# Performance work log

Measured on AMD Instinct MI355X. Metric: run time of the kernel, lower is better.

## Reference

```python
import jax, jax.numpy as jnp
import numpy as np

N_STEPS = 2048; WINDOW = [4, 4, 4]; INNER = 5
D_MODEL = 128; N_HEADS = 4; D_K = D_MODEL // N_HEADS
D_FFN = 512; N_LAYERS = 2; D_BOT = D_MODEL // 4; BATCH = 2
NEG = -1e9


def _mask_and_sizes():
    # faithful port of Pyraformer get_mask
    all_size = [N_STEPS]
    for w in WINDOW:
        all_size.append(all_size[-1] // w)
    S = sum(all_size)
    m = np.zeros((S, S), np.float32)
    inner = INNER // 2
    starts = [0]
    for sz in all_size:
        starts.append(starts[-1] + sz)
    for li, sz in enumerate(all_size):
        s = starts[li]
        for i in range(s, s + sz):
            m[i, max(i - inner, s):min(i + inner + 1, s + sz)] = 1
    for li in range(1, len(all_size)):
        s = starts[li]
        for i in range(s, s + all_size[li]):
            left = (s - all_size[li - 1]) + (i - s) * WINDOW[li - 1]
            right = s if i == s + all_size[li] - 1 else (s - all_size[li - 1]) + (i - s + 1) * WINDOW[li - 1]
            m[i, left:right] = 1
            m[left:right, i] = 1
    return (1 - m).astype(bool), all_size  # True = masked out


def _refer_points(all_size):
    # faithful port of Pyraformer refer_points -> [n_steps, n_levels]
    idx = np.zeros((N_STEPS, len(all_size)), np.int32)
    for i in range(N_STEPS):
        idx[i, 0] = i
        former = i
        for j in range(1, len(all_size)):
            start = int(sum(all_size[:j]))
            inner_idx = former - (start - all_size[j - 1])
            former = start + min(inner_idx // WINDOW[j - 1], all_size[j] - 1)
            idx[i, j] = former
    return idx


def _ln(x, g, b, eps):
    mu = jnp.mean(x, -1, keepdims=True)
    var = jnp.mean((x - mu) ** 2, -1, keepdims=True)
    return (x - mu) * jax.lax.rsqrt(var + eps) * g + b


def setup_inputs() -> dict:
    key = jax.random.key(0)
    ks = jax.random.split(key, 12)
    mask_np, all_size = _mask_and_sizes()
    idx_np = _refer_points(all_size)
    s = 0.02
    rn = lambda k, shape: jax.random.normal(k, shape, jnp.float32) * s
    L, W = N_LAYERS, len(WINDOW)
    return {
        'x': jax.random.normal(ks[0], (BATCH, N_STEPS, D_MODEL), jnp.float32),
        'w_down': rn(ks[1], (D_MODEL, D_BOT)), 'b_down': jnp.zeros((D_BOT,)),
        'conv_w': rn(ks[2], (W, D_BOT, D_BOT, WINDOW[0])), 'conv_b': jnp.zeros((W, D_BOT)),
        'bn_g': jnp.ones((W, D_BOT)), 'bn_b': jnp.zeros((W, D_BOT)),
        'bn_m': jnp.zeros((W, D_BOT)), 'bn_v': jnp.ones((W, D_BOT)),
        'w_up': rn(ks[3], (D_BOT, D_MODEL)), 'b_up': jnp.zeros((D_MODEL,)),
        'ln0_g': jnp.ones((D_MODEL,)), 'ln0_b': jnp.zeros((D_MODEL,)),
        'wq': rn(ks[4], (L, D_MODEL, N_HEADS * D_K)), 'wk': rn(ks[5], (L, D_MODEL, N_HEADS * D_K)),
        'wv': rn(ks[6], (L, D_MODEL, N_HEADS * D_K)), 'wo': rn(ks[7], (L, N_HEADS * D_K, D_MODEL)),
        'ln1_g': jnp.ones((L, D_MODEL)), 'ln1_b': jnp.zeros((L, D_MODEL)),
        'ffn_w1': rn(ks[8], (L, D_MODEL, D_FFN)), 'ffn_b1': jnp.zeros((L, D_FFN)),
        'ffn_w2': rn(ks[9], (L, D_FFN, D_MODEL)), 'ffn_b2': jnp.zeros((L, D_MODEL)),
        'ln2_g': jnp.ones((L, D_MODEL)), 'ln2_b': jnp.zeros((L, D_MODEL)),
        'mask': jnp.asarray(mask_np), 'indexes': jnp.asarray(idx_np),
    }


def _fwd(mask, indexes, x, w_down, b_down, conv_w, conv_b, bn_g, bn_b, bn_m, bn_v,
         w_up, b_up, ln0_g, ln0_b, wq, wk, wv, wo, ln1_g, ln1_b,
         ffn_w1, ffn_b1, ffn_w2, ffn_b2, ln2_g, ln2_b):
    B = x.shape[0]
    # Bottleneck_Construct: down-proj, strided convs per scale, up-proj, concat, LN
    t = (x @ w_down + b_down).transpose(0, 2, 1)  # [B, d_bot, N]
    outs = []
    for i in range(len(WINDOW)):
        t = jax.lax.conv_general_dilated(t, conv_w[i], (WINDOW[i],), 'VALID',
                                         dimension_numbers=('NCH', 'OIH', 'NCH'))
        t = t + conv_b[i][None, :, None]
        t = (t - bn_m[i][None, :, None]) * jax.lax.rsqrt(bn_v[i][None, :, None] + 1e-5) \
            * bn_g[i][None, :, None] + bn_b[i][None, :, None]  # BatchNorm1d (eval)
        t = jax.nn.elu(t)
        outs.append(t)
    pooled = jnp.concatenate(outs, axis=2).transpose(0, 2, 1)  # [B, 672, d_bot]
    h = jnp.concatenate([x, pooled @ w_up + b_up], axis=1)  # [B, S=2720, d_model]
    h = _ln(h, ln0_g, ln0_b, 1e-5)
    S = h.shape[1]
    mask4 = mask[None, None]  # [1,1,S,S], True = masked
    inv_temp = 1.0 / np.float32(np.sqrt(D_K))
    for l in range(N_LAYERS):
        q = (h @ wq[l]).reshape(B, S, N_HEADS, D_K).transpose(0, 2, 1, 3)
        k = (h @ wk[l]).reshape(B, S, N_HEADS, D_K).transpose(0, 2, 1, 3)
        v = (h @ wv[l]).reshape(B, S, N_HEADS, D_K).transpose(0, 2, 1, 3)
        attn = jnp.einsum('bhqd,bhkd->bhqk', q * inv_temp, k)
        attn = jnp.where(mask4, NEG, attn)
        attn = jax.nn.softmax(attn, axis=-1)
        o = jnp.einsum('bhqk,bhkd->bhqd', attn, v).transpose(0, 2, 1, 3).reshape(B, S, N_HEADS * D_K)
        h = _ln(h + o @ wo[l], ln1_g[l], ln1_b[l], 1e-6)
        f = jax.nn.relu(h @ ffn_w1[l] + ffn_b1[l]) @ ffn_w2[l] + ffn_b2[l]
        h = _ln(h + f, ln2_g[l], ln2_b[l], 1e-6)
    # multi-scale gather reassembly (refer_points)
    idx_flat = indexes.reshape(-1)  # [n_steps * n_levels]
    all_enc = h[:, idx_flat, :]  # [B, n_steps*levels, d_model]
    return all_enc.reshape(B, N_STEPS, -1)  # [B, n_steps, levels*d_model]


def reference(x, mask, indexes, w_down, b_down, conv_w, conv_b, bn_g, bn_b, bn_m, bn_v,
              w_up, b_up, ln0_g, ln0_b, wq, wk, wv, wo, ln1_g, ln1_b,
              ffn_w1, ffn_b1, ffn_w2, ffn_b2, ln2_g, ln2_b):
    return _fwd(mask, indexes, x, w_down, b_down, conv_w, conv_b, bn_g, bn_b, bn_m, bn_v,
                w_up, b_up, ln0_g, ln0_b, wq, wk, wv, wo, ln1_g, ln1_b,
                ffn_w1, ffn_b1, ffn_w2, ffn_b2, ln2_g, ln2_b)
```

## Files before the change

### kernel.cpp

```cpp
#include <hip/hip_runtime.h>
#include <hip/hip_bf16.h>

#define S_TOT 2720

typedef short bf16x8 __attribute__((ext_vector_type(8)));
typedef float f32x4 __attribute__((ext_vector_type(4)));

__device__ __forceinline__ float bf2f(short u) {
    return __uint_as_float(((unsigned int)(unsigned short)u) << 16);
}

__global__ void prep_kernel(const float* __restrict__ w1, const float* __restrict__ w2,
                            const float* __restrict__ wq, const float* __restrict__ wk,
                            const float* __restrict__ wv, const float* __restrict__ wo,
                            __hip_bfloat16* __restrict__ out,
                            const float* __restrict__ x, const float* __restrict__ wd,
                            const float* __restrict__ bd, float* __restrict__ t0) {
    int id = blockIdx.x * 256 + threadIdx.x;
    if (id < 131072) {
        int l = id >> 16, r = id & 65535;
        int j = r >> 7, k = r & 127;
        out[id] = __float2bfloat16(w1[l * 65536 + k * 512 + j]);
    } else if (id < 262144) {
        int t = id - 131072;
        int l = t >> 16, r = t & 65535;
        int d = r >> 9, j = r & 511;
        out[id] = __float2bfloat16(w2[l * 65536 + j * 128 + d]);
    } else if (id < 360448) {
        int t = id - 262144;
        int l = t / 49152, r = t % 49152;
        int m = r >> 14, rr = r & 16383;
        int j = rr >> 7, k = rr & 127;
        const float* W = (m == 0) ? wq : (m == 1) ? wk : wv;
        out[id] = __float2bfloat16(W[l * 16384 + k * 128 + j]);
    } else if (id < 393216) {
        int t = id - 360448;
        int l = t >> 14, r = t & 16383;
        int j = r >> 7, k = r & 127;
        out[id] = __float2bfloat16(wo[l * 16384 + k * 128 + j]);
    } else {
        int did = id - 393216;
        int c = did & 31;
        int r = did >> 5;
        const float* xr = x + (size_t)r * 128;
        float a0 = bd[c], a1 = 0.f, a2 = 0.f, a3 = 0.f;
#pragma unroll
        for (int k = 0; k < 128; k += 4) {
            a0 += xr[k]     * wd[(k)     * 32 + c];
            a1 += xr[k + 1] * wd[(k + 1) * 32 + c];
            a2 += xr[k + 2] * wd[(k + 2) * 32 + c];
            a3 += xr[k + 3] * wd[(k + 3) * 32 + c];
        }
        t0[did] = (a0 + a1) + (a2 + a3);
    }
}

__global__ void conv_kernel(const float* __restrict__ in, float* __restrict__ pooled,
                            const float* __restrict__ cw, const float* __restrict__ cb,
                            const float* __restrict__ bg, const float* __restrict__ bb,
                            const float* __restrict__ bm, const float* __restrict__ bv,
                            int level, int in_bstride, int in_off, int Lout, int out_off,
                            int total) {
    int id = blockIdx.x * 256 + threadIdx.x;
    if (id >= total) return;
    int co = id & 31;
    int lo = (id >> 5) % Lout;
    int b  = id / (32 * Lout);
    const float* ib = in + (size_t)(b * in_bstride + in_off + lo * 4) * 32;
    const float* w  = cw + (size_t)(level * 32 + co) * 32 * 4;
    float acc0 = 0.f, acc1 = 0.f, acc2 = 0.f, acc3 = 0.f;
#pragma unroll
    for (int ci = 0; ci < 32; ++ci) {
        acc0 += ib[0 * 32 + ci] * w[ci * 4 + 0];
        acc1 += ib[1 * 32 + ci] * w[ci * 4 + 1];
        acc2 += ib[2 * 32 + ci] * w[ci * 4 + 2];
        acc3 += ib[3 * 32 + ci] * w[ci * 4 + 3];
    }
    float acc = ((acc0 + acc1) + (acc2 + acc3)) + cb[level * 32 + co];
    acc = (acc - bm[level * 32 + co]) * rsqrtf(bv[level * 32 + co] + 1e-5f)
          * bg[level * 32 + co] + bb[level * 32 + co];
    acc = acc > 0.f ? acc : expm1f(acc);
    pooled[(size_t)(b * 672 + out_off + lo) * 32 + co] = acc;
}

__global__ void build_ln_kernel(const float* __restrict__ x, const float* __restrict__ pooled,
                                const float* __restrict__ w_up, const float* __restrict__ b_up,
                                const float* __restrict__ g, const float* __restrict__ bta,
                                float* __restrict__ h) {
    int wave = threadIdx.x >> 6;
    int lane = threadIdx.x & 63;
    int row = blockIdx.x * 4 + wave;
    int b = row / S_TOT, s = row % S_TOT;
    float v0, v1;
    if (s < 2048) {
        const float* xr = x + (size_t)(b * 2048 + s) * 128;
        v0 = xr[lane]; v1 = xr[lane + 64];
    } else {
        int p = s - 2048;
        const float* pr = pooled + (size_t)(b * 672 + p) * 32;
        float a0 = b_up[lane], a1 = b_up[lane + 64];
        float a2 = 0.f, a3 = 0.f;
#pragma unroll
        for (int k = 0; k < 32; k += 2) {
            float p0 = pr[k], p1 = pr[k + 1];
            a0 += p0 * w_up[k * 128 + lane];
            a1 += p0 * w_up[k * 128 + lane + 64];
            a2 += p1 * w_up[(k + 1) * 128 + lane];
            a3 += p1 * w_up[(k + 1) * 128 + lane + 64];
        }
        v0 = a0 + a2; v1 = a1 + a3;
    }
    float sum = v0 + v1;
#pragma unroll
    for (int off = 32; off; off >>= 1) sum += __shfl_xor(sum, off);
    float mu = sum * (1.f / 128.f);
    float d0 = v0 - mu, d1 = v1 - mu;
    float vs = d0 * d0 + d1 * d1;
#pragma unroll
    for (int off = 32; off; off >>= 1) vs += __shfl_xor(vs, off);
    float inv = rsqrtf(vs * (1.f / 128.f) + 1e-5f);
    h[(size_t)row * 128 + lane]      = d0 * inv * g[lane]      + bta[lane];
    h[(size_t)row * 128 + lane + 64] = d1 * inv * g[lane + 64] + bta[lane + 64];
}

__global__ __launch_bounds__(256) void qkv_mfma_kernel(const float* __restrict__ H,
                                                       const __hip_bfloat16* __restrict__ wqkvt,
                                                       __hip_bfloat16* __restrict__ q,
                                                       __hip_bfloat16* __restrict__ k,
                                                       __hip_bfloat16* __restrict__ v) {
    __shared__ __hip_bfloat16 hsb[16][136];
    int tid = threadIdx.x;
    int r0 = blockIdx.x * 16;
    {
        int row = tid >> 4, c0 = (tid & 15) * 8;
        const float* src = &H[(size_t)(r0 + row) * 128 + c0];
        float4 x0 = *(const float4*)src;
        float4 x1 = *(const float4*)(src + 4);
        __hip_bfloat16* d = &hsb[row][c0];
        d[0] = __float2bfloat16(x0.x); d[1] = __float2bfloat16(x0.y);
        d[2] = __float2bfloat16(x0.z); d[3] = __float2bfloat16(x0.w);
        d[4] = __float2bfloat16(x1.x); d[5] = __float2bfloat16(x1.y);
        d[6] = __float2bfloat16(x1.z); d[7] = __float2bfloat16(x1.w);
    }
    __syncthreads();
    int lane = tid & 63, wv = tid >> 6;
    int l15 = lane & 15, grp = lane >> 4;
    bf16x8 afr[4];
#pragma unroll
    for (int ks = 0; ks < 4; ++ks)
        afr[ks] = *(const bf16x8*)&hsb[l15][ks * 32 + grp * 8];
    __hip_bfloat16* O[3] = {q, k, v};
#pragma unroll
    for (int t = 0; t < 6; ++t) {
        int gt = wv * 6 + t;
        int mat = gt >> 3, jj = gt & 7;
        int j0 = jj * 16;
        f32x4 acc = {0.f, 0.f, 0.f, 0.f};
        const __hip_bfloat16* wb = &wqkvt[(size_t)(mat * 128 + j0 + l15) * 128 + grp * 8];
#pragma unroll
        for (int ks = 0; ks < 4; ++ks) {
            bf16x8 bfr = *(const bf16x8*)&wb[ks * 32];
            acc = __builtin_amdgcn_mfma_f32_16x16x32_bf16(afr[ks], bfr, acc, 0, 0, 0);
        }
        __hip_bfloat16* Om = O[mat];
#pragma unroll
        for (int i = 0; i < 4; ++i)
            Om[(size_t)(r0 + grp * 4 + i) * 128 + j0 + l15] = __float2bfloat16(acc[i]);
    }
}

__global__ __launch_bounds__(256) void attn_o_ffn_kernel(const __hip_bfloat16* __restrict__ Q,
                                                         const __hip_bfloat16* __restrict__ K,
                                                         const __hip_bfloat16* __restrict__ V,
                                                         const __hip_bfloat16* __restrict__ wot,
                                                         const float* __restrict__ g1,
                                                         const float* __restrict__ b1ta,
                                                         const __hip_bfloat16* __restrict__ w1t,
                                                         const float* __restrict__ b1,
                                                         const __hip_bfloat16* __restrict__ w2t,
                                                         const float* __restrict__ b2,
                                                         const float* __restrict__ g2,
                                                         const float* __restrict__ b2ta,
                                                         float* __restrict__ h) {
    __shared__ __hip_bfloat16 osb[16][136];
    __shared__ __hip_bfloat16 pb[16][520];
    __shared__ float partf[16][128];
    __shared__ float h1s[16][128];
    int tid = threadIdx.x;
    int r0 = blockIdx.x * 16;
    {
        int rl = tid >> 4;
        int hh = (tid >> 2) & 3;
        int qd = tid & 3;
        int d0 = qd * 8;
        int row = r0 + rl;
        int b = row / S_TOT, i = row % S_TOT;
        int li, s;
        if (i < 2048)      { li = 0; s = 0;    }
        else if (i < 2560) { li = 1; s = 2048; }
        else if (i < 2688) { li = 2; s = 2560; }
        else               { li = 3; s = 2688; }
        int sz = (li == 0) ? 2048 : (li == 1) ? 512 : (li == 2) ? 128 : 32;
        int pstart = (li == 0) ? 2048 : (li == 1) ? 2560 : 2688;
        int cstart = (li == 1) ? 0 : (li == 2) ? 2048 : 2560;

        bf16x8 qv = *(const bf16x8*)(Q + (size_t)row * 128 + hh * 32 + d0);
        float qf[8];
#pragma unroll
        for (int e = 0; e < 8; ++e) qf[e] = bf2f(qv[e]);
        const float invt = 0.17677669529663687f;

        float sc[10];
        int   nj[10];
        bool  vl[10];
#pragma unroll
        for (int slot = 0; slot < 10; ++slot) {
            int j; bool valid;
            if (slot < 5)       { j = i - 2 + slot;                         valid = (j >= s) && (j < s + sz); }
            else if (slot == 5) { j = pstart + ((i - s) >> 2);              valid = (li < 3); }
            else                { j = cstart + ((i - s) << 2) + (slot - 6); valid = (li > 0); }
            nj[slot] = j; vl[slot] = valid;
            float dot = 0.f;
            if (valid) {
                bf16x8 kv = *(const bf16x8*)(K + (size_t)(b * S_TOT + j) * 128 + hh * 32 + d0);
#pragma unroll
                for (int e = 0; e < 8; ++e) dot += qf[e] * bf2f(kv[e]);
            }
            dot += __shfl_xor(dot, 1);
            dot += __shfl_xor(dot, 2);
            sc[slot] = valid ? dot * invt : -1e30f;
        }
        float mx = sc[0];
#pragma unroll
        for (int slot = 1; slot < 10; ++slot) mx = fmaxf(mx, sc[slot]);
        float ssum = 0.f;
#pragma unroll
        for (int slot = 0; slot < 10; ++slot) { sc[slot] = __expf(sc[slot] - mx); ssum += sc[slot]; }
        float rinv = 1.f / ssum;
        float oacc[8];
#pragma unroll
        for (int e = 0; e < 8; ++e) oacc[e] = 0.f;
#pragma unroll
        for (int slot = 0; slot < 10; ++slot) {
            if (vl[slot]) {
                float p = sc[slot] * rinv;
                bf16x8 vv = *(const bf16x8*)(V + (size_t)(b * S_TOT + nj[slot]) * 128 + hh * 32 + d0);
#pragma unroll
                for (int e = 0; e < 8; ++e) oacc[e] += p * bf2f(vv[e]);
            }
        }
        __hip_bfloat16* dst = &osb[rl][hh * 32 + d0];
#pragma unroll
        for (int e = 0; e < 8; ++e) dst[e] = __float2bfloat16(oacc[e]);
    }
    __syncthreads();
    int lane = tid & 63, wv = tid >> 6;
    int l15 = lane & 15, grp = lane >> 4;
    {
        bf16x8 afr[4];
#pragma unroll
        for (int ks = 0; ks < 4; ++ks)
            afr[ks] = *(const bf16x8*)&osb[l15][ks * 32 + grp * 8];
#pragma unroll
        for (int t = 0; t < 2; ++t) {
            int j0 = (wv * 2 + t) * 16;
            f32x4 acc = {0.f, 0.f, 0.f, 0.f};
            const __hip_bfloat16* wb = &wot[(size_t)(j0 + l15) * 128 + grp * 8];
#pragma unroll
            for (int ks = 0; ks < 4; ++ks) {
                bf16x8 bfr = *(const bf16x8*)&wb[ks * 32];
                acc = __builtin_amdgcn_mfma_f32_16x16x32_bf16(afr[ks], bfr, acc, 0, 0, 0);
            }
#pragma unroll
            for (int i = 0; i < 4; ++i)
                partf[grp * 4 + i][j0 + l15] = acc[i];
        }
    }
    __syncthreads();
    {
        int r = tid >> 4, d0 = (tid & 15) * 8;
        size_t row = (size_t)(r0 + r) * 128;
        float vv[8];
        float sum = 0.f;
#pragma unroll
        for (int i = 0; i < 8; ++i) {
            int d = d0 + i;
            vv[i] = partf[r][d] + h[row + d];
            sum += vv[i];
        }
#pragma unroll
        for (int off = 8; off; off >>= 1) sum += __shfl_xor(sum, off);
        float mu = sum * (1.f / 128.f);
        float vs = 0.f;
#pragma unroll
        for (int i = 0; i < 8; ++i) { vv[i] -= mu; vs += vv[i] * vv[i]; }
#pragma unroll
        for (int off = 8; off; off >>= 1) vs += __shfl_xor(vs, off);
        float inv = rsqrtf(vs * (1.f / 128.f) + 1e-6f);
        __hip_bfloat16* db = &osb[r][d0];
#pragma unroll
        for (int i = 0; i < 8; ++i) {
            float hv = vv[i] * inv * g1[d0 + i] + b1ta[d0 + i];
            h1s[r][d0 + i] = hv;
            db[i] = __float2bfloat16(hv);
        }
    }
    __syncthreads();
    {
        bf16x8 afr[4];
#pragma unroll
        for (int ks = 0; ks < 4; ++ks)
            afr[ks] = *(const bf16x8*)&osb[l15][ks * 32 + grp * 8];
#pragma unroll
        for (int t = 0; t < 8; ++t) {
            int j0 = (wv * 8 + t) * 16;
            f32x4 acc = {0.f, 0.f, 0.f, 0.f};
            const __hip_bfloat16* wb = &w1t[(size_t)(j0 + l15) * 128 + grp * 8];
#pragma unroll
            for (int ks = 0; ks < 4; ++ks) {
                bf16x8 bfr = *(const bf16x8*)&wb[ks * 32];
                acc = __builtin_amdgcn_mfma_f32_16x16x32_bf16(afr[ks], bfr, acc, 0, 0, 0);
            }
            float bv = b1[j0 + l15];
#pragma unroll
            for (int i = 0; i < 4; ++i)
                pb[grp * 4 + i][j0 + l15] = __float2bfloat16(fmaxf(acc[i] + bv, 0.f));
        }
    }
    __syncthreads();
    {
        f32x4 acc2a = {0.f, 0.f, 0.f, 0.f};
        f32x4 acc2b = {0.f, 0.f, 0.f, 0.f};
        const __hip_bfloat16* wb0 = &w2t[(size_t)(wv * 32 + l15) * 512 + grp * 8];
        const __hip_bfloat16* wb1 = &w2t[(size_t)(wv * 32 + 16 + l15) * 512 + grp * 8];
#pragma unroll
        for (int ks = 0; ks < 16; ++ks) {
            bf16x8 afr2 = *(const bf16x8*)&pb[l15][ks * 32 + grp * 8];
            bf16x8 b0 = *(const bf16x8*)&wb0[ks * 32];
            bf16x8 b1f = *(const bf16x8*)&wb1[ks * 32];
            acc2a = __builtin_amdgcn_mfma_f32_16x16x32_bf16(afr2, b0, acc2a, 0, 0, 0);
            acc2b = __builtin_amdgcn_mfma_f32_16x16x32_bf16(afr2, b1f, acc2b, 0, 0, 0);
        }
#pragma unroll
        for (int i = 0; i < 4; ++i) {
            partf[grp * 4 + i][wv * 32 + l15]      = acc2a[i];
            partf[grp * 4 + i][wv * 32 + 16 + l15] = acc2b[i];
        }
    }
    __syncthreads();
    {
        int r = tid >> 4, d0 = (tid & 15) * 8;
        size_t row = (size_t)(r0 + r) * 128;
        float vv[8];
        float sum = 0.f;
#pragma unroll
        for (int i = 0; i < 8; ++i) {
            int d = d0 + i;
            vv[i] = partf[r][d] + b2[d] + h1s[r][d];
            sum += vv[i];
        }
#pragma unroll
        for (int off = 8; off; off >>= 1) sum += __shfl_xor(sum, off);
        float mu = sum * (1.f / 128.f);
        float vs = 0.f;
#pragma unroll
        for (int i = 0; i < 8; ++i) { vv[i] -= mu; vs += vv[i] * vv[i]; }
#pragma unroll
        for (int off = 8; off; off >>= 1) vs += __shfl_xor(vs, off);
        float inv = rsqrtf(vs * (1.f / 128.f) + 1e-6f);
#pragma unroll
        for (int i = 0; i < 8; ++i) vv[i] = vv[i] * inv * g2[d0 + i] + b2ta[d0 + i];
        *(float4*)&h[row + d0]     = make_float4(vv[0], vv[1], vv[2], vv[3]);
        *(float4*)&h[row + d0 + 4] = make_float4(vv[4], vv[5], vv[6], vv[7]);
    }
}

__global__ void gather_kernel(const float* __restrict__ H, const int* __restrict__ idx,
                              float* __restrict__ out) {
    int id = blockIdx.x * 256 + threadIdx.x;
    int d4 = id & 31;
    int j = (id >> 5) & 3;
    int t = (id >> 7) & 2047;
    int b = id >> 18;
    int src = idx[t * 4 + j];
    ((float4*)out)[id] = *(const float4*)&H[((size_t)(b * S_TOT + src) * 128) + d4 * 4];
}

extern "C" void kernel_launch(void* const* d_in, const int* in_sizes, int n_in,
                              void* d_out, int out_size, void* d_ws, size_t ws_size,
                              hipStream_t stream) {
    (void)in_sizes; (void)n_in; (void)out_size; (void)ws_size;
    const float* x       = (const float*)d_in[0];
    const float* w_down  = (const float*)d_in[1];
    const float* b_down  = (const float*)d_in[2];
    const float* conv_w  = (const float*)d_in[3];
    const float* conv_b  = (const float*)d_in[4];
    const float* bn_g    = (const float*)d_in[5];
    const float* bn_b    = (const float*)d_in[6];
    const float* bn_m    = (const float*)d_in[7];
    const float* bn_v    = (const float*)d_in[8];
    const float* w_up    = (const float*)d_in[9];
    const float* b_up    = (const float*)d_in[10];
    const float* ln0_g   = (const float*)d_in[11];
    const float* ln0_b   = (const float*)d_in[12];
    const float* wq      = (const float*)d_in[13];
    const float* wk      = (const float*)d_in[14];
    const float* wv      = (const float*)d_in[15];
    const float* wo      = (const float*)d_in[16];
    const float* ln1_g   = (const float*)d_in[17];
    const float* ln1_b   = (const float*)d_in[18];
    const float* ffn_w1  = (const float*)d_in[19];
    const float* ffn_b1  = (const float*)d_in[20];
    const float* ffn_w2  = (const float*)d_in[21];
    const float* ffn_b2  = (const float*)d_in[22];
    const float* ln2_g   = (const float*)d_in[23];
    const float* ln2_b   = (const float*)d_in[24];
    const int* indexes   = (const int*)d_in[26];

    float* ws = (float*)d_ws;
    float* t0     = ws;
    float* pooled = ws + 131072;
    float* h      = ws + 174080;
    __hip_bfloat16* qb = (__hip_bfloat16*)(ws + 870400);
    __hip_bfloat16* kb = (__hip_bfloat16*)(ws + 1218560);
    __hip_bfloat16* vb = (__hip_bfloat16*)(ws + 1566720);
    __hip_bfloat16* wb_all = (__hip_bfloat16*)(ws + 1914880);
    __hip_bfloat16* w1t   = wb_all;
    __hip_bfloat16* w2t   = wb_all + 131072;
    __hip_bfloat16* wqkvt = wb_all + 262144;
    __hip_bfloat16* wot   = wb_all + 360448;

    prep_kernel<<<2048, 256, 0, stream>>>(ffn_w1, ffn_w2, wq, wk, wv, wo, wb_all,
                                          x, w_down, b_down, t0);
    conv_kernel<<<128, 256, 0, stream>>>(t0, pooled, conv_w, conv_b, bn_g, bn_b, bn_m, bn_v,
                                         0, 2048, 0, 512, 0, 32768);
    conv_kernel<<<32, 256, 0, stream>>>(pooled, pooled, conv_w, conv_b, bn_g, bn_b, bn_m, bn_v,
                                        1, 672, 0, 128, 512, 8192);
    conv_kernel<<<8, 256, 0, stream>>>(pooled, pooled, conv_w, conv_b, bn_g, bn_b, bn_m, bn_v,
                                       2, 672, 512, 32, 640, 2048);
    build_ln_kernel<<<1360, 256, 0, stream>>>(x, pooled, w_up, b_up, ln0_g, ln0_b, h);

    for (int l = 0; l < 2; ++l) {
        qkv_mfma_kernel<<<340, 256, 0, stream>>>(h, wqkvt + l * 49152, qb, kb, vb);
        attn_o_ffn_kernel<<<340, 256, 0, stream>>>(qb, kb, vb, wot + l * 16384,
                                                   ln1_g + l * 128, ln1_b + l * 128,
                                                   w1t + l * 65536, ffn_b1 + l * 512,
                                                   w2t + l * 65536, ffn_b2 + l * 128,
                                                   ln2_g + l * 128, ln2_b + l * 128, h);
    }
    gather_kernel<<<2048, 256, 0, stream>>>(h, indexes, (float*)d_out);
}
```

Measured before the change: 115.7 us.

## Fuse small conv levels and fuse build-LN into first QKV projection

Merges the second and third pyramid conv levels into a single two-block kernel that keeps the intermediate level in shared memory. Fuses the input build and LayerNorm step into the first layer's QKV MFMA kernel, so the normalized rows feed the projection directly without re-reading h. This removes several kernel launches and a global round trip. The fused conv kernel runs on only two blocks with long serial loops, which may lengthen that stage.

```diff
diff --git a/kernel.cpp b/kernel.cpp
--- a/kernel.cpp
+++ b/kernel.cpp
@@ -83,44 +83,145 @@
     pooled[(size_t)(b * 672 + out_off + lo) * 32 + co] = acc;
 }
 
-__global__ void build_ln_kernel(const float* __restrict__ x, const float* __restrict__ pooled,
-                                const float* __restrict__ w_up, const float* __restrict__ b_up,
-                                const float* __restrict__ g, const float* __restrict__ bta,
-                                float* __restrict__ h) {
-    int wave = threadIdx.x >> 6;
-    int lane = threadIdx.x & 63;
-    int row = blockIdx.x * 4 + wave;
-    int b = row / S_TOT, s = row % S_TOT;
-    float v0, v1;
-    if (s < 2048) {
-        const float* xr = x + (size_t)(b * 2048 + s) * 128;
-        v0 = xr[lane]; v1 = xr[lane + 64];
-    } else {
-        int p = s - 2048;
-        const float* pr = pooled + (size_t)(b * 672 + p) * 32;
-        float a0 = b_up[lane], a1 = b_up[lane + 64];
-        float a2 = 0.f, a3 = 0.f;
-#pragma unroll
-        for (int k = 0; k < 32; k += 2) {
-            float p0 = pr[k], p1 = pr[k + 1];
-            a0 += p0 * w_up[k * 128 + lane];
-            a1 += p0 * w_up[k * 128 + lane + 64];
-            a2 += p1 * w_up[(k + 1) * 128 + lane];
-            a3 += p1 * w_up[(k + 1) * 128 + lane + 64];
-        }
-        v0 = a0 + a2; v1 = a1 + a3;
-    }
-    float sum = v0 + v1;
-#pragma unroll
-    for (int off = 32; off; off >>= 1) sum += __shfl_xor(sum, off);
-    float mu = sum * (1.f / 128.f);
-    float d0 = v0 - mu, d1 = v1 - mu;
-    float vs = d0 * d0 + d1 * d1;
-#pragma unroll
-    for (int off = 32; off; off >>= 1) vs += __shfl_xor(vs, off);
-    float inv = rsqrtf(vs * (1.f / 128.f) + 1e-5f);
-    h[(size_t)row * 128 + lane]      = d0 * inv * g[lane]      + bta[lane];
-    h[(size_t)row * 128 + lane + 64] = d1 * inv * g[lane + 64] + bta[lane + 64];
+__global__ __launch_bounds__(256) void conv23_kernel(float* __restrict__ pooled,
+                                                     const float* __restrict__ cw,
+                                                     const float* __restrict__ cb,
+                                                     const float* __restrict__ bg,
+                                                     const float* __restrict__ bb,
+                                                     const float* __restrict__ bm,
+                                                     const float* __restrict__ bv) {
+    __shared__ float c2s[128][32];
+    int b = blockIdx.x;
+    int tid = threadIdx.x;
+#pragma unroll
+    for (int t = 0; t < 16; ++t) {
+        int oid = tid + t * 256;
+        int co = oid & 31, lo = oid >> 5;
+        const float* ib = pooled + (size_t)(b * 672 + lo * 4) * 32;
+        const float* w  = cw + (size_t)(32 + co) * 128;
+        float a0 = 0.f, a1 = 0.f, a2 = 0.f, a3 = 0.f;
+#pragma unroll
+        for (int ci = 0; ci < 32; ++ci) {
+            a0 += ib[0 * 32 + ci] * w[ci * 4 + 0];
+            a1 += ib[1 * 32 + ci] * w[ci * 4 + 1];
+            a2 += ib[2 * 32 + ci] * w[ci * 4 + 2];
+            a3 += ib[3 * 32 + ci] * w[ci * 4 + 3];
+        }
+        float acc = ((a0 + a1) + (a2 + a3)) + cb[32 + co];
+        acc = (acc - bm[32 + co]) * rsqrtf(bv[32 + co] + 1e-5f) * bg[32 + co] + bb[32 + co];
+        acc = acc > 0.f ? acc : expm1f(acc);
+        c2s[lo][co] = acc;
+        pooled[(size_t)(b * 672 + 512 + lo) * 32 + co] = acc;
+    }
+    __syncthreads();
+#pragma unroll
+    for (int t = 0; t < 4; ++t) {
+        int oid = tid + t * 256;
+        int co = oid & 31, lo = oid >> 5;
+        const float* w = cw + (size_t)(64 + co) * 128;
+        float a0 = 0.f, a1 = 0.f, a2 = 0.f, a3 = 0.f;
+#pragma unroll
+        for (int ci = 0; ci < 32; ++ci) {
+            a0 += c2s[lo * 4 + 0][ci] * w[ci * 4 + 0];
+            a1 += c2s[lo * 4 + 1][ci] * w[ci * 4 + 1];
+            a2 += c2s[lo * 4 + 2][ci] * w[ci * 4 + 2];
+            a3 += c2s[lo * 4 + 3][ci] * w[ci * 4 + 3];
+        }
+        float acc = ((a0 + a1) + (a2 + a3)) + cb[64 + co];
+        acc = (acc - bm[64 + co]) * rsqrtf(bv[64 + co] + 1e-5f) * bg[64 + co] + bb[64 + co];
+        acc = acc > 0.f ? acc : expm1f(acc);
+        pooled[(size_t)(b * 672 + 640 + lo) * 32 + co] = acc;
+    }
+}
+
+__global__ __launch_bounds__(256) void build_qkv_kernel(const float* __restrict__ x,
+                                                        const float* __restrict__ pooled,
+                                                        const float* __restrict__ w_up,
+                                                        const float* __restrict__ b_up,
+                                                        const float* __restrict__ g,
+                                                        const float* __restrict__ bta,
+                                                        const __hip_bfloat16* __restrict__ wqkvt,
+                                                        float* __restrict__ h,
+                                                        __hip_bfloat16* __restrict__ q,
+                                                        __hip_bfloat16* __restrict__ k,
+                                                        __hip_bfloat16* __restrict__ v) {
+    __shared__ __hip_bfloat16 hsb[16][136];
+    int tid = threadIdx.x;
+    int r0 = blockIdx.x * 16;
+    {
+        int rl = tid >> 4, c0 = (tid & 15) * 8;
+        int row = r0 + rl;
+        int b = row / S_TOT, s = row % S_TOT;
+        float vv[8];
+        if (s < 2048) {
+            const float* xr = x + (size_t)(b * 2048 + s) * 128 + c0;
+            float4 x0 = *(const float4*)xr;
+            float4 x1 = *(const float4*)(xr + 4);
+            vv[0] = x0.x; vv[1] = x0.y; vv[2] = x0.z; vv[3] = x0.w;
+            vv[4] = x1.x; vv[5] = x1.y; vv[6] = x1.z; vv[7] = x1.w;
+        } else {
+            int p = s - 2048;
+            const float* pr = pooled + (size_t)(b * 672 + p) * 32;
+#pragma unroll
+            for (int i = 0; i < 8; ++i) vv[i] = b_up[c0 + i];
+#pragma unroll
+            for (int kk = 0; kk < 32; ++kk) {
+                float pv = pr[kk];
+                const float* wr = w_up + kk * 128 + c0;
+                float4 w0 = *(const float4*)wr;
+                float4 w1v = *(const float4*)(wr + 4);
+                vv[0] += pv * w0.x; vv[1] += pv * w0.y; vv[2] += pv * w0.z; vv[3] += pv * w0.w;
+                vv[4] += pv * w1v.x; vv[5] += pv * w1v.y; vv[6] += pv * w1v.z; vv[7] += pv * w1v.w;
+            }
+        }
+        float sum = 0.f;
+#pragma unroll
+        for (int i = 0; i < 8; ++i) sum += vv[i];
+#pragma unroll
+        for (int off = 8; off; off >>= 1) sum += __shfl_xor(sum, off);
+        float mu = sum * (1.f / 128.f);
+        float vs = 0.f;
+#pragma unroll
+        for (int i = 0; i < 8; ++i) { vv[i] -= mu; vs += vv[i] * vv[i]; }
+#pragma unroll
+        for (int off = 8; off; off >>= 1) vs += __shfl_xor(vs, off);
+        float inv = rsqrtf(vs * (1.f / 128.f) + 1e-5f);
+        size_t hrow = (size_t)row * 128;
+        __hip_bfloat16* db = &hsb[rl][c0];
+#pragma unroll
+        for (int i = 0; i < 8; ++i) {
+            float hv = vv[i] * inv * g[c0 + i] + bta[c0 + i];
+            vv[i] = hv;
+            db[i] = __float2bfloat16(hv);
+        }
+        *(float4*)&h[hrow + c0]     = make_float4(vv[0], vv[1], vv[2], vv[3]);
+        *(float4*)&h[hrow + c0 + 4] = make_float4(vv[4], vv[5], vv[6], vv[7]);
+    }
+    __syncthreads();
+    int lane = tid & 63, wv = tid >> 6;
+    int l15 = lane & 15, grp = lane >> 4;
+    bf16x8 afr[4];
+#pragma unroll
+    for (int ks = 0; ks < 4; ++ks)
+        afr[ks] = *(const bf16x8*)&hsb[l15][ks * 32 + grp * 8];
+    __hip_bfloat16* O[3] = {q, k, v};
+#pragma unroll
+    for (int t = 0; t < 6; ++t) {
+        int gt = wv * 6 + t;
+        int mat = gt >> 3, jj = gt & 7;
+        int j0 = jj * 16;
+        f32x4 acc = {0.f, 0.f, 0.f, 0.f};
+        const __hip_bfloat16* wb = &wqkvt[(size_t)(mat * 128 + j0 + l15) * 128 + grp * 8];
+#pragma unroll
+        for (int ks = 0; ks < 4; ++ks) {
+            bf16x8 bfr = *(const bf16x8*)&wb[ks * 32];
+            acc = __builtin_amdgcn_mfma_f32_16x16x32_bf16(afr[ks], bfr, acc, 0, 0, 0);
+        }
+        __hip_bfloat16* Om = O[mat];
+#pragma unroll
+        for (int i = 0; i < 4; ++i)
+            Om[(size_t)(r0 + grp * 4 + i) * 128 + j0 + l15] = __float2bfloat16(acc[i]);
+    }
 }
 
 __global__ __launch_bounds__(256) void qkv_mfma_kernel(const float* __restrict__ H,
@@ -244,9 +345,9 @@
         for (int slot = 0; slot < 10; ++slot) {
             if (vl[slot]) {
                 float p = sc[slot] * rinv;
-                bf16x8 vv = *(const bf16x8*)(V + (size_t)(b * S_TOT + nj[slot]) * 128 + hh * 32 + d0);
-#pragma unroll
-                for (int e = 0; e < 8; ++e) oacc[e] += p * bf2f(vv[e]);
+                bf16x8 vvb = *(const bf16x8*)(V + (size_t)(b * S_TOT + nj[slot]) * 128 + hh * 32 + d0);
+#pragma unroll
+                for (int e = 0; e < 8; ++e) oacc[e] += p * bf2f(vvb[e]);
             }
         }
         __hip_bfloat16* dst = &osb[rl][hh * 32 + d0];
@@ -434,19 +535,19 @@
                                           x, w_down, b_down, t0);
     conv_kernel<<<128, 256, 0, stream>>>(t0, pooled, conv_w, conv_b, bn_g, bn_b, bn_m, bn_v,
                                          0, 2048, 0, 512, 0, 32768);
-    conv_kernel<<<32, 256, 0, stream>>>(pooled, pooled, conv_w, conv_b, bn_g, bn_b, bn_m, bn_v,
-                                        1, 672, 0, 128, 512, 8192);
-    conv_kernel<<<8, 256, 0, stream>>>(pooled, pooled, conv_w, conv_b, bn_g, bn_b, bn_m, bn_v,
-                                       2, 672, 512, 32, 640, 2048);
-    build_ln_kernel<<<1360, 256, 0, stream>>>(x, pooled, w_up, b_up, ln0_g, ln0_b, h);
-
-    for (int l = 0; l < 2; ++l) {
-        qkv_mfma_kernel<<<340, 256, 0, stream>>>(h, wqkvt + l * 49152, qb, kb, vb);
-        attn_o_ffn_kernel<<<340, 256, 0, stream>>>(qb, kb, vb, wot + l * 16384,
-                                                   ln1_g + l * 128, ln1_b + l * 128,
-                                                   w1t + l * 65536, ffn_b1 + l * 512,
-                                                   w2t + l * 65536, ffn_b2 + l * 128,
-                                                   ln2_g + l * 128, ln2_b + l * 128, h);
-    }
+    conv23_kernel<<<2, 256, 0, stream>>>(pooled, conv_w, conv_b, bn_g, bn_b, bn_m, bn_v);
+    build_qkv_kernel<<<340, 256, 0, stream>>>(x, pooled, w_up, b_up, ln0_g, ln0_b,
+                                              wqkvt, h, qb, kb, vb);
+    attn_o_ffn_kernel<<<340, 256, 0, stream>>>(qb, kb, vb, wot,
+                                               ln1_g, ln1_b,
+                                               w1t, ffn_b1,
+                                               w2t, ffn_b2,
+                                               ln2_g, ln2_b, h);
+    qkv_mfma_kernel<<<340, 256, 0, stream>>>(h, wqkvt + 49152, qb, kb, vb);
+    attn_o_ffn_kernel<<<340, 256, 0, stream>>>(qb, kb, vb, wot + 16384,
+                                               ln1_g + 128, ln1_b + 128,
+                                               w1t + 65536, ffn_b1 + 512,
+                                               w2t + 65536, ffn_b2 + 128,
+                                               ln2_g + 128, ln2_b + 128, h);
     gather_kernel<<<2048, 256, 0, stream>>>(h, indexes, (float*)d_out);
 }
```

New measurement: 192.4 us. 1.66x slower.
